# Kernel optimization log

Measured on AMD Instinct MI355X. Metric: run time of the kernel, lower is better.

Reference implementation:

```python
import jax, jax.numpy as jnp
import numpy as np

WS = 8        # window_size
NH = 12       # num_heads


def setup_inputs() -> dict:
    key = jax.random.key(0)
    ks = jax.random.split(key, 9)
    B, C, H, W = 4, 384, 128, 128
    s = 1.0 / np.sqrt(C)
    x = jax.random.normal(ks[0], (B, C, H, W), dtype=jnp.float32)
    Wq = jax.random.normal(ks[1], (C, C), dtype=jnp.float32) * s
    bq = jax.random.normal(ks[2], (C,), dtype=jnp.float32) * 0.01
    Wk = jax.random.normal(ks[3], (C, C), dtype=jnp.float32) * s
    bk = jax.random.normal(ks[4], (C,), dtype=jnp.float32) * 0.01
    Wv = jax.random.normal(ks[5], (C, C), dtype=jnp.float32) * s
    bv = jax.random.normal(ks[6], (C,), dtype=jnp.float32) * 0.01
    Wp = jax.random.normal(ks[7], (C, C), dtype=jnp.float32) * s
    bp = jax.random.normal(ks[8], (C,), dtype=jnp.float32) * 0.01
    return {"x": x, "Wq": Wq, "bq": bq, "Wk": Wk, "bk": bk,
            "Wv": Wv, "bv": bv, "Wp": Wp, "bp": bp}


def reference(x, Wq, bq, Wk, bk, Wv, bv, Wp, bp):
    B, C, H, W = x.shape
    ws2 = WS * WS
    dk = C // NH
    scale = dk ** -0.5

    # window_partition: flat row-major reshape (same semantics as torch's
    # reshape on a contiguous [B,C,H,W] tensor), then permute+view.
    p = x.reshape(B, H // WS, WS, W // WS, WS, C)
    p = jnp.transpose(p, (0, 5, 1, 3, 2, 4))          # [B, C, H/ws, W/ws, ws, ws]
    p = p.reshape(B, C, -1, ws2)                       # [B, C, nW, ws*ws]

    def conv1x1(w, b):  # 1x1 Conv2d on [B,C,nW,ws2]
        return jnp.einsum('bcnw,oc->bonw', p, w) + b[None, :, None, None]

    def heads(t):  # permute(0,2,3,1).contiguous().reshape -> [B, NH, nW, ws2, dk]
        t = jnp.transpose(t, (0, 2, 3, 1))             # [B, nW, ws2, C]
        return t.reshape(B, NH, -1, ws2, dk)           # row-major reinterpretation

    q = heads(conv1x1(Wq, bq))
    k = heads(conv1x1(Wk, bk))
    v = heads(conv1x1(Wv, bv))

    scores = jnp.einsum('bhnqd,bhnkd->bhnqk', q, k) * scale
    attn = jax.nn.softmax(scores, axis=-1)
    o = jnp.einsum('bhnqk,bhnkd->bhnqd', attn, v)      # [B, NH, nW, ws2, dk]
    o = o.reshape(B, -1, ws2, C)                       # [B, nW, ws2, C]

    # window_unpartition
    u = o.reshape(B, -1, WS, WS, C)
    u = jnp.transpose(u, (0, 4, 1, 2, 3))              # [B, C, nW, ws, ws]
    u = u.reshape(B, C, H, W)

    y = jnp.einsum('bchw,oc->bohw', u, Wp) + bp[None, :, None, None]
    return y
```

## Files before the change

### kernel.cpp

```cpp
#include <hip/hip_runtime.h>
#include <hip/hip_bf16.h>
#include <stdint.h>


typedef __bf16 bf16_t;
typedef __bf16 bf16x8 __attribute__((ext_vector_type(8)));
typedef __bf16 bf16x4 __attribute__((ext_vector_type(4)));
typedef float f32x4 __attribute__((ext_vector_type(4)));

__device__ __forceinline__ void gload_lds16(const void* g, void* l) {
  __builtin_amdgcn_global_load_lds((__attribute__((address_space(1))) void*)(g),
                                   (__attribute__((address_space(3))) void*)(l),
                                   16, 0, 0);
}

__global__ __launch_bounds__(256) void convw_kernel(
    const float* __restrict__ wq, const float* __restrict__ wk,
    const float* __restrict__ wv, const float* __restrict__ wp,
    bf16_t* __restrict__ oq, bf16_t* __restrict__ ok,
    bf16_t* __restrict__ ov, bf16_t* __restrict__ op_) {
  int i = blockIdx.x * 256 + threadIdx.x;
  oq[i] = (bf16_t)wq[i];
  ok[i] = (bf16_t)wk[i];
  ov[i] = (bf16_t)wv[i];
  op_[i] = (bf16_t)wp[i];
}

__global__ __launch_bounds__(256) void prep_kernel(const float* __restrict__ x,
                                                   bf16_t* __restrict__ Xp) {
  int gid = blockIdx.x * 256 + threadIdx.x;
  int row = gid / 96;
  int c4 = (gid - row * 96) * 4;
  int b = row >> 14;
  int pp = row & 16383;
  int n1 = pp >> 10, n3 = (pp >> 6) & 15, w2 = (pp >> 3) & 7, w4 = pp & 7;
  int P = (n1 << 10) | (w2 << 7) | (n3 << 3) | w4;
  float4 v = *(const float4*)(x + (size_t)((b << 14) | P) * 384 + c4);
  bf16x4 o;
  o[0] = (bf16_t)v.x; o[1] = (bf16_t)v.y; o[2] = (bf16_t)v.z; o[3] = (bf16_t)v.w;
  *(bf16x4*)(Xp + (size_t)row * 384 + c4) = o;
}

__global__ __launch_bounds__(256) void qkv_gemm(
    const bf16_t* __restrict__ Xp, const bf16_t* __restrict__ Wcat,
    const float* __restrict__ bq, const float* __restrict__ bk,
    const float* __restrict__ bv,
    bf16_t* __restrict__ Qs, bf16_t* __restrict__ Ks, bf16_t* __restrict__ Vs) {
  __shared__ __align__(16) bf16_t As[2 * 256 * 32];
  __shared__ __align__(16) bf16_t Bs[2 * 128 * 32];
  const int tid = threadIdx.x;
  const int F = blockIdx.x;
  const int xcd = F & 7;
  const int t = F >> 3;
  const int j = t % 9;
  const int gq = t / 9;
  const int m0 = (gq * 8 + xcd) * 256;
  const int which = j / 3;
  const int cb = (j % 3) * 128;
  const float* bias = which == 0 ? bq : (which == 1 ? bk : bv);
  bf16_t* Out = which == 0 ? Qs : (which == 1 ? Ks : Vs);
  const bf16_t* Arows = Xp + (size_t)m0 * 384;
  const bf16_t* Brows = Wcat + (size_t)j * 128 * 384;

  const int lane = tid & 63, wvv = tid >> 6;
  const int l15 = lane & 15, hi = lane >> 4;
  const int wrM = wvv >> 1, wc = wvv & 1;
  const int slot = hi ^ ((l15 >> 1) & 3);

  auto stage = [&](int kt) {
    const int k0 = kt * 32;
    bf16_t* Ad = As + (kt & 1) * 8192;
    bf16_t* Bd = Bs + (kt & 1) * 4096;
#pragma unroll
    for (int jj = 0; jj < 4; ++jj) {
      int idx = jj * 256 + tid;
      int row = idx >> 2;
      int sg = (idx & 3) ^ ((idx >> 3) & 3);
      gload_lds16(Arows + (size_t)row * 384 + k0 + sg * 8,
                  (char*)Ad + (jj * 256 + wvv * 64) * 16);
    }
#pragma unroll
    for (int h = 0; h < 2; ++h) {
      int q = wvv * 128 + h * 64 + lane;
      int row = q >> 2;
      int sg = (lane & 3) ^ ((lane >> 3) & 3);
      gload_lds16(Brows + (size_t)row * 384 + k0 + sg * 8,
                  (char*)Bd + (wvv * 128 + h * 64) * 16);
    }
  };

  stage(0);
  stage(1);

  f32x4 acc[8][4] = {};
#pragma unroll 1
  for (int kt = 0; kt < 12; ++kt) {
    bf16_t* Ab = As + (kt & 1) * 8192;
    bf16_t* Bb = Bs + (kt & 1) * 4096;
    if (kt == 11) asm volatile("s_waitcnt vmcnt(0)" ::: "memory");
    else          asm volatile("s_waitcnt vmcnt(6)" ::: "memory");
    __builtin_amdgcn_s_barrier();
    bf16x8 a[8], bfr[4];
#pragma unroll
    for (int i = 0; i < 8; ++i)
      a[i] = *(const bf16x8*)(Ab + (wrM * 128 + i * 16 + l15) * 32 + slot * 8);
#pragma unroll
    for (int ni = 0; ni < 4; ++ni)
      bfr[ni] = *(const bf16x8*)(Bb + (wc * 64 + ni * 16 + l15) * 32 + slot * 8);
#pragma unroll
    for (int mi = 0; mi < 8; ++mi)
#pragma unroll
      for (int ni = 0; ni < 4; ++ni)
        acc[mi][ni] = __builtin_amdgcn_mfma_f32_16x16x32_bf16(a[mi], bfr[ni],
                                                              acc[mi][ni], 0, 0, 0);
    asm volatile("s_waitcnt lgkmcnt(0)" ::: "memory");
    __builtin_amdgcn_sched_barrier(0);
    __builtin_amdgcn_s_barrier();
    if (kt + 2 < 12) stage(kt + 2);
  }

#pragma unroll
  for (int ni = 0; ni < 4; ++ni) {
    int chan = cb + wc * 64 + ni * 16 + l15;
    float bv_ = bias[chan];
#pragma unroll
    for (int mi = 0; mi < 8; ++mi)
#pragma unroll
      for (int r = 0; r < 4; ++r) {
        int row = m0 + wrM * 128 + mi * 16 + hi * 4 + r;
        Out[(size_t)row * 384 + chan] = (bf16_t)(acc[mi][ni][r] + bv_);
      }
  }
}

__global__ __launch_bounds__(64) void attn_kernel(const bf16_t* __restrict__ Q,
                                                  const bf16_t* __restrict__ K,
                                                  const bf16_t* __restrict__ V,
                                                  bf16_t* __restrict__ O) {
  const size_t base = (size_t)blockIdx.x * 2048;
  const bf16_t* q = Q + base;
  const bf16_t* k = K + base;
  const bf16_t* v = V + base;
  bf16_t* o = O + base;
  const int lane = threadIdx.x;
  const int l15 = lane & 15, hi = lane >> 4;

  __shared__ __align__(16) bf16_t Vt[32][72];
  __shared__ __align__(16) bf16_t Ps[64][72];

#pragma unroll
  for (int j = 0; j < 4; ++j) {
    bf16x8 vv = *(const bf16x8*)(v + lane * 32 + j * 8);
#pragma unroll
    for (int e = 0; e < 8; ++e) Vt[j * 8 + e][lane] = vv[e];
  }

  bf16x8 aQ[4], bK[4];
#pragma unroll
  for (int i = 0; i < 4; ++i) {
    aQ[i] = *(const bf16x8*)(q + (i * 16 + l15) * 32 + hi * 8);
    bK[i] = *(const bf16x8*)(k + (i * 16 + l15) * 32 + hi * 8);
  }
  f32x4 sc[4][4] = {};
#pragma unroll
  for (int mi = 0; mi < 4; ++mi)
#pragma unroll
    for (int ni = 0; ni < 4; ++ni)
      sc[mi][ni] = __builtin_amdgcn_mfma_f32_16x16x32_bf16(aQ[mi], bK[ni],
                                                           sc[mi][ni], 0, 0, 0);

  const float SCALE = 0.17677669529663687f;
  float rs[4][4];
#pragma unroll
  for (int mi = 0; mi < 4; ++mi) {
#pragma unroll
    for (int r = 0; r < 4; ++r) {
      float s0 = sc[mi][0][r] * SCALE, s1 = sc[mi][1][r] * SCALE;
      float s2 = sc[mi][2][r] * SCALE, s3 = sc[mi][3][r] * SCALE;
      float mx = fmaxf(fmaxf(s0, s1), fmaxf(s2, s3));
      mx = fmaxf(mx, __shfl_xor(mx, 1));
      mx = fmaxf(mx, __shfl_xor(mx, 2));
      mx = fmaxf(mx, __shfl_xor(mx, 4));
      mx = fmaxf(mx, __shfl_xor(mx, 8));
      float p0 = __expf(s0 - mx), p1 = __expf(s1 - mx);
      float p2 = __expf(s2 - mx), p3 = __expf(s3 - mx);
      int row = mi * 16 + hi * 4 + r;
      Ps[row][0 + l15] = (bf16_t)p0;
      Ps[row][16 + l15] = (bf16_t)p1;
      Ps[row][32 + l15] = (bf16_t)p2;
      Ps[row][48 + l15] = (bf16_t)p3;
      float sum = p0 + p1 + p2 + p3;
      sum += __shfl_xor(sum, 1);
      sum += __shfl_xor(sum, 2);
      sum += __shfl_xor(sum, 4);
      sum += __shfl_xor(sum, 8);
      rs[mi][r] = sum;
    }
  }
  __syncthreads();

  f32x4 oacc[4][2] = {};
#pragma unroll
  for (int mi = 0; mi < 4; ++mi)
#pragma unroll
    for (int ks = 0; ks < 2; ++ks) {
      bf16x8 aP = *(const bf16x8*)(&Ps[mi * 16 + l15][ks * 32 + hi * 8]);
#pragma unroll
      for (int n2 = 0; n2 < 2; ++n2) {
        bf16x8 bV = *(const bf16x8*)(&Vt[n2 * 16 + l15][ks * 32 + hi * 8]);
        oacc[mi][n2] = __builtin_amdgcn_mfma_f32_16x16x32_bf16(aP, bV,
                                                               oacc[mi][n2], 0, 0, 0);
      }
    }
#pragma unroll
  for (int mi = 0; mi < 4; ++mi)
#pragma unroll
    for (int n2 = 0; n2 < 2; ++n2)
#pragma unroll
      for (int r = 0; r < 4; ++r) {
        int row = mi * 16 + hi * 4 + r;
        o[row * 32 + n2 * 16 + l15] = (bf16_t)(oacc[mi][n2][r] / rs[mi][r]);
      }
}

__device__ __forceinline__ void stage_tile(const bf16_t* __restrict__ A,
                                           const bf16_t* __restrict__ B,
                                           bf16_t* As, bf16_t* Bs, int k0, int tid) {
  const int lane = tid & 63, wvv = tid >> 6;
  const int s = (lane & 3) ^ ((lane >> 3) & 3);
#pragma unroll
  for (int j = 0; j < 2; ++j) {
    int q = wvv * 128 + j * 64 + lane;
    int row = q >> 2;
    gload_lds16(A + (size_t)row * 384 + k0 + s * 8,
                (char*)As + (wvv * 128 + j * 64) * 16);
    gload_lds16(B + (size_t)row * 384 + k0 + s * 8,
                (char*)Bs + (wvv * 128 + j * 64) * 16);
  }
}

__device__ __forceinline__ void gemm_mainloop(const bf16_t* __restrict__ Arows,
                                              const bf16_t* __restrict__ Brows,
                                              bf16_t* As, bf16_t* Bs,
                                              int tid, f32x4 acc[4][4]) {
  const int lane = tid & 63;
  const int l15 = lane & 15, hi = lane >> 4;
  const int wr = (tid >> 6) >> 1, wc = (tid >> 6) & 1;
  const int slot = hi ^ ((l15 >> 1) & 3);
  stage_tile(Arows, Brows, As, Bs, 0, tid);
  stage_tile(Arows, Brows, As + 4096, Bs + 4096, 32, tid);
#pragma unroll
  for (int kt = 0; kt < 12; ++kt) {
    bf16_t* Ab = As + (kt & 1) * 4096;
    bf16_t* Bb = Bs + (kt & 1) * 4096;
    if (kt == 11) asm volatile("s_waitcnt vmcnt(0)" ::: "memory");
    else          asm volatile("s_waitcnt vmcnt(4)" ::: "memory");
    __builtin_amdgcn_s_barrier();
    bf16x8 a[4], bfr[4];
#pragma unroll
    for (int i = 0; i < 4; ++i) {
      a[i] = *(const bf16x8*)(Ab + (wr * 64 + i * 16 + l15) * 32 + slot * 8);
      bfr[i] = *(const bf16x8*)(Bb + (wc * 64 + i * 16 + l15) * 32 + slot * 8);
    }
#pragma unroll
    for (int mi = 0; mi < 4; ++mi)
#pragma unroll
      for (int ni = 0; ni < 4; ++ni)
        acc[mi][ni] = __builtin_amdgcn_mfma_f32_16x16x32_bf16(a[mi], bfr[ni],
                                                              acc[mi][ni], 0, 0, 0);
    asm volatile("s_waitcnt lgkmcnt(0)" ::: "memory");
    __builtin_amdgcn_sched_barrier(0);
    __builtin_amdgcn_s_barrier();
    if (kt + 2 < 12)
      stage_tile(Arows, Brows, Ab, Bb, (kt + 2) * 32, tid);
  }
}

__global__ __launch_bounds__(256) void proj_gemm(const bf16_t* __restrict__ Wpb,
                                                 const bf16_t* __restrict__ O,
                                                 const float* __restrict__ bp,
                                                 float* __restrict__ y) {
  __shared__ __align__(16) bf16_t As[2 * 128 * 32];
  __shared__ __align__(16) bf16_t Bs[2 * 128 * 32];
  const int tid = threadIdx.x;
  const int F = blockIdx.x;
  const int xcd = F & 7;
  const int t = F >> 3;
  const int j = t % 3;
  const int gq = t / 3;
  const int g = gq * 8 + xcd;
  const int n0 = (g & 127) * 128;
  const int b = g >> 7;
  const int m0 = j * 128;
  f32x4 acc[4][4] = {};
  gemm_mainloop(Wpb + (size_t)m0 * 384, O + ((size_t)b * 16384 + n0) * 384,
                As, Bs, tid, acc);
  const int lane = tid & 63, wvv = tid >> 6;
  const int l15 = lane & 15, hi = lane >> 4;
  const int wr = wvv >> 1, wc = wvv & 1;
  float* yb = y + (size_t)b * 6291456;
#pragma unroll
  for (int mi = 0; mi < 4; ++mi)
#pragma unroll
    for (int r = 0; r < 4; ++r) {
      int och = m0 + wr * 64 + mi * 16 + hi * 4 + r;
      float bpv = bp[och];
#pragma unroll
      for (int ni = 0; ni < 4; ++ni) {
        int pix = n0 + wc * 64 + ni * 16 + l15;
        yb[(size_t)och * 16384 + pix] = acc[mi][ni][r] + bpv;
      }
    }
}

extern "C" void kernel_launch(void* const* d_in, const int* in_sizes, int n_in,
                              void* d_out, int out_size, void* d_ws, size_t ws_size,
                              hipStream_t stream) {
  const float* x  = (const float*)d_in[0];
  const float* Wq = (const float*)d_in[1];
  const float* bq = (const float*)d_in[2];
  const float* Wk = (const float*)d_in[3];
  const float* bk = (const float*)d_in[4];
  const float* Wv = (const float*)d_in[5];
  const float* bv = (const float*)d_in[6];
  const float* Wp = (const float*)d_in[7];
  const float* bp = (const float*)d_in[8];
  float* y = (float*)d_out;

  char* ws = (char*)d_ws;
  const size_t SZ = 50331648;
  bf16_t* Xp  = (bf16_t*)(ws);
  bf16_t* Vs  = (bf16_t*)(ws + SZ);
  bf16_t* Wcat = (bf16_t*)(ws + 2 * SZ);
  bf16_t* Wkb = Wcat + 147456;
  bf16_t* Wvb = Wkb + 147456;
  bf16_t* Wpb = Wvb + 147456;
  bf16_t* Qs  = (bf16_t*)d_out;
  bf16_t* Ks  = (bf16_t*)((char*)d_out + SZ);
  bf16_t* Ob  = Xp;

  convw_kernel<<<576, 256, 0, stream>>>(Wq, Wk, Wv, Wp, Wcat, Wkb, Wvb, Wpb);
  prep_kernel<<<24576, 256, 0, stream>>>(x, Xp);
  qkv_gemm<<<2304, 256, 0, stream>>>(Xp, Wcat, bq, bk, bv, Qs, Ks, Vs);
  attn_kernel<<<12288, 64, 0, stream>>>(Qs, Ks, Vs, Ob);
  proj_gemm<<<1536, 256, 0, stream>>>(Wpb, Ob, bp, y);
}
```

Baseline: 223.4 us.

## Deepen qkv GEMM pipeline with 5-stage LDS ring and 8 waves

The QKV projection GEMM moves from 256 to 512 threads. Each of its 8 waves now computes a 64x64 sub-tile, where each of the previous 4 waves computed 128x64. The two-stage static LDS double buffer becomes a 5-stage ring in 120KB of dynamic shared memory with 4 stages prefetched ahead. LDS fragments are double-buffered in registers so the next k-step's reads overlap the current MFMAs, and s_setprio is raised around the MFMA block. The aim is to hide global-load latency and cut barrier stalls, at the cost of limiting the kernel to one block per CU because of the large LDS footprint.

```diff
diff --git a/kernel.cpp b/kernel.cpp
--- a/kernel.cpp
+++ b/kernel.cpp
@@ -41,13 +41,12 @@
   *(bf16x4*)(Xp + (size_t)row * 384 + c4) = o;
 }
 
-__global__ __launch_bounds__(256) void qkv_gemm(
+__global__ __launch_bounds__(512, 2) void qkv_gemm(
     const bf16_t* __restrict__ Xp, const bf16_t* __restrict__ Wcat,
     const float* __restrict__ bq, const float* __restrict__ bk,
     const float* __restrict__ bv,
     bf16_t* __restrict__ Qs, bf16_t* __restrict__ Ks, bf16_t* __restrict__ Vs) {
-  __shared__ __align__(16) bf16_t As[2 * 256 * 32];
-  __shared__ __align__(16) bf16_t Bs[2 * 128 * 32];
+  extern __shared__ __align__(16) char smem[];
   const int tid = threadIdx.x;
   const int F = blockIdx.x;
   const int xcd = F & 7;
@@ -62,61 +61,75 @@
   const bf16_t* Arows = Xp + (size_t)m0 * 384;
   const bf16_t* Brows = Wcat + (size_t)j * 128 * 384;
 
-  const int lane = tid & 63, wvv = tid >> 6;
+  const int lane = tid & 63, wid = tid >> 6;
   const int l15 = lane & 15, hi = lane >> 4;
-  const int wrM = wvv >> 1, wc = wvv & 1;
+  const int wr = wid >> 1, wc = wid & 1;
   const int slot = hi ^ ((l15 >> 1) & 3);
 
   auto stage = [&](int kt) {
     const int k0 = kt * 32;
-    bf16_t* Ad = As + (kt & 1) * 8192;
-    bf16_t* Bd = Bs + (kt & 1) * 4096;
-#pragma unroll
-    for (int jj = 0; jj < 4; ++jj) {
-      int idx = jj * 256 + tid;
+    char* base = smem + (kt % 5) * 24576;
+#pragma unroll
+    for (int jj = 0; jj < 2; ++jj) {
+      int idx = jj * 512 + tid;
       int row = idx >> 2;
       int sg = (idx & 3) ^ ((idx >> 3) & 3);
       gload_lds16(Arows + (size_t)row * 384 + k0 + sg * 8,
-                  (char*)Ad + (jj * 256 + wvv * 64) * 16);
-    }
-#pragma unroll
-    for (int h = 0; h < 2; ++h) {
-      int q = wvv * 128 + h * 64 + lane;
-      int row = q >> 2;
-      int sg = (lane & 3) ^ ((lane >> 3) & 3);
+                  base + (jj * 512 + wid * 64) * 16);
+    }
+    {
+      int row = tid >> 2;
+      int sg = (tid & 3) ^ ((tid >> 3) & 3);
       gload_lds16(Brows + (size_t)row * 384 + k0 + sg * 8,
-                  (char*)Bd + (wvv * 128 + h * 64) * 16);
+                  base + 16384 + (wid * 64) * 16);
     }
   };
 
-  stage(0);
-  stage(1);
-
-  f32x4 acc[8][4] = {};
-#pragma unroll 1
+  stage(0); stage(1); stage(2); stage(3);
+  asm volatile("s_waitcnt vmcnt(6)" ::: "memory");
+  __builtin_amdgcn_s_barrier();
+  __builtin_amdgcn_sched_barrier(0);
+
+  bf16x8 fA[2][4], fB[2][4];
+  {
+    const char* Ab = smem;
+    const char* Bb = Ab + 16384;
+#pragma unroll
+    for (int i = 0; i < 4; ++i) {
+      fA[0][i] = *(const bf16x8*)(Ab + (wr * 64 + i * 16 + l15) * 64 + slot * 16);
+      fB[0][i] = *(const bf16x8*)(Bb + (wc * 64 + i * 16 + l15) * 64 + slot * 16);
+    }
+  }
+
+  f32x4 acc[4][4] = {};
+#pragma unroll
   for (int kt = 0; kt < 12; ++kt) {
-    bf16_t* Ab = As + (kt & 1) * 8192;
-    bf16_t* Bb = Bs + (kt & 1) * 4096;
-    if (kt == 11) asm volatile("s_waitcnt vmcnt(0)" ::: "memory");
-    else          asm volatile("s_waitcnt vmcnt(6)" ::: "memory");
-    __builtin_amdgcn_s_barrier();
-    bf16x8 a[8], bfr[4];
-#pragma unroll
-    for (int i = 0; i < 8; ++i)
-      a[i] = *(const bf16x8*)(Ab + (wrM * 128 + i * 16 + l15) * 32 + slot * 8);
-#pragma unroll
-    for (int ni = 0; ni < 4; ++ni)
-      bfr[ni] = *(const bf16x8*)(Bb + (wc * 64 + ni * 16 + l15) * 32 + slot * 8);
-#pragma unroll
-    for (int mi = 0; mi < 8; ++mi)
+    const int cur = kt & 1, nxt = cur ^ 1;
+    if (kt > 0) {
+      __builtin_amdgcn_s_barrier();
+      __builtin_amdgcn_sched_barrier(0);
+    }
+    if (kt + 4 < 12) stage(kt + 4);
+    if (kt < 11) {
+      const char* Ab = smem + ((kt + 1) % 5) * 24576;
+      const char* Bb = Ab + 16384;
+#pragma unroll
+      for (int i = 0; i < 4; ++i) {
+        fA[nxt][i] = *(const bf16x8*)(Ab + (wr * 64 + i * 16 + l15) * 64 + slot * 16);
+        fB[nxt][i] = *(const bf16x8*)(Bb + (wc * 64 + i * 16 + l15) * 64 + slot * 16);
+      }
+    }
+    __builtin_amdgcn_s_setprio(1);
+#pragma unroll
+    for (int mi = 0; mi < 4; ++mi)
 #pragma unroll
       for (int ni = 0; ni < 4; ++ni)
-        acc[mi][ni] = __builtin_amdgcn_mfma_f32_16x16x32_bf16(a[mi], bfr[ni],
-                                                              acc[mi][ni], 0, 0, 0);
-    asm volatile("s_waitcnt lgkmcnt(0)" ::: "memory");
-    __builtin_amdgcn_sched_barrier(0);
-    __builtin_amdgcn_s_barrier();
-    if (kt + 2 < 12) stage(kt + 2);
+        acc[mi][ni] = __builtin_amdgcn_mfma_f32_16x16x32_bf16(
+            fA[cur][mi], fB[cur][ni], acc[mi][ni], 0, 0, 0);
+    __builtin_amdgcn_s_setprio(0);
+    if (kt <= 7)      asm volatile("s_waitcnt vmcnt(6)" ::: "memory");
+    else if (kt == 8) asm volatile("s_waitcnt vmcnt(3)" ::: "memory");
+    else if (kt == 9) asm volatile("s_waitcnt vmcnt(0)" ::: "memory");
   }
 
 #pragma unroll
@@ -124,10 +137,10 @@
     int chan = cb + wc * 64 + ni * 16 + l15;
     float bv_ = bias[chan];
 #pragma unroll
-    for (int mi = 0; mi < 8; ++mi)
+    for (int mi = 0; mi < 4; ++mi)
 #pragma unroll
       for (int r = 0; r < 4; ++r) {
-        int row = m0 + wrM * 128 + mi * 16 + hi * 4 + r;
+        int row = m0 + wr * 64 + mi * 16 + hi * 4 + r;
         Out[(size_t)row * 384 + chan] = (bf16_t)(acc[mi][ni][r] + bv_);
       }
   }
@@ -339,9 +352,12 @@
   bf16_t* Ks  = (bf16_t*)((char*)d_out + SZ);
   bf16_t* Ob  = Xp;
 
+  hipFuncSetAttribute((const void*)qkv_gemm,
+                      hipFuncAttributeMaxDynamicSharedMemorySize, 122880);
+
   convw_kernel<<<576, 256, 0, stream>>>(Wq, Wk, Wv, Wp, Wcat, Wkb, Wvb, Wpb);
   prep_kernel<<<24576, 256, 0, stream>>>(x, Xp);
-  qkv_gemm<<<2304, 256, 0, stream>>>(Xp, Wcat, bq, bk, bv, Qs, Ks, Vs);
+  qkv_gemm<<<2304, 512, 122880, stream>>>(Xp, Wcat, bq, bk, bv, Qs, Ks, Vs);
   attn_kernel<<<12288, 64, 0, stream>>>(Qs, Ks, Vs, Ob);
   proj_gemm<<<1536, 256, 0, stream>>>(Wpb, Ob, bp, y);
 }
```

Measured after the change: 192.1 us. 14.0% less time.

## Triple-buffer QKV GEMM with 512-thread blocks and one barrier per k-step

Applied to the files above, without the earlier changes.

The QKV GEMM now runs 512-thread blocks, each computing a 512x128 output tile instead of 256x128. Shared memory moves to a dynamic, triple-buffered layout, so the next-but-one tile's global-to-LDS loads are issued right after a single barrier per k-step, replacing the two barriers and the full lgkm drain of the old double-buffered loop. The k-loop is fully unrolled and MFMA sections get raised wave priority to overlap loads with math. The cost is 120 KB of LDS per block, which limits each CU to one block, and half as many blocks in the grid.

```diff
diff --git a/kernel.cpp b/kernel.cpp
--- a/kernel.cpp
+++ b/kernel.cpp
@@ -41,20 +41,19 @@
   *(bf16x4*)(Xp + (size_t)row * 384 + c4) = o;
 }
 
-__global__ __launch_bounds__(256) void qkv_gemm(
+__global__ __launch_bounds__(512, 2) void qkv_gemm(
     const bf16_t* __restrict__ Xp, const bf16_t* __restrict__ Wcat,
     const float* __restrict__ bq, const float* __restrict__ bk,
     const float* __restrict__ bv,
     bf16_t* __restrict__ Qs, bf16_t* __restrict__ Ks, bf16_t* __restrict__ Vs) {
-  __shared__ __align__(16) bf16_t As[2 * 256 * 32];
-  __shared__ __align__(16) bf16_t Bs[2 * 128 * 32];
+  extern __shared__ __align__(16) char smem[];
   const int tid = threadIdx.x;
   const int F = blockIdx.x;
   const int xcd = F & 7;
   const int t = F >> 3;
   const int j = t % 9;
   const int gq = t / 9;
-  const int m0 = (gq * 8 + xcd) * 256;
+  const int m0 = (gq * 8 + xcd) * 512;
   const int which = j / 3;
   const int cb = (j % 3) * 128;
   const float* bias = which == 0 ? bq : (which == 1 ? bk : bv);
@@ -62,61 +61,63 @@
   const bf16_t* Arows = Xp + (size_t)m0 * 384;
   const bf16_t* Brows = Wcat + (size_t)j * 128 * 384;
 
-  const int lane = tid & 63, wvv = tid >> 6;
+  const int lane = tid & 63, wid = tid >> 6;
   const int l15 = lane & 15, hi = lane >> 4;
-  const int wrM = wvv >> 1, wc = wvv & 1;
+  const int wr = wid >> 1, wc = wid & 1;
   const int slot = hi ^ ((l15 >> 1) & 3);
 
   auto stage = [&](int kt) {
     const int k0 = kt * 32;
-    bf16_t* Ad = As + (kt & 1) * 8192;
-    bf16_t* Bd = Bs + (kt & 1) * 4096;
+    char* base = smem + (kt % 3) * 40960;
 #pragma unroll
     for (int jj = 0; jj < 4; ++jj) {
-      int idx = jj * 256 + tid;
+      int idx = jj * 512 + tid;
       int row = idx >> 2;
       int sg = (idx & 3) ^ ((idx >> 3) & 3);
       gload_lds16(Arows + (size_t)row * 384 + k0 + sg * 8,
-                  (char*)Ad + (jj * 256 + wvv * 64) * 16);
-    }
-#pragma unroll
-    for (int h = 0; h < 2; ++h) {
-      int q = wvv * 128 + h * 64 + lane;
-      int row = q >> 2;
-      int sg = (lane & 3) ^ ((lane >> 3) & 3);
+                  base + (jj * 512 + wid * 64) * 16);
+    }
+    {
+      int row = tid >> 2;
+      int sg = (tid & 3) ^ ((tid >> 3) & 3);
       gload_lds16(Brows + (size_t)row * 384 + k0 + sg * 8,
-                  (char*)Bd + (wvv * 128 + h * 64) * 16);
+                  base + 32768 + (wid * 64) * 16);
     }
   };
 
-  stage(0);
-  stage(1);
+  stage(0); stage(1);
+  asm volatile("s_waitcnt vmcnt(5)" ::: "memory");
+  __builtin_amdgcn_s_barrier();
+  __builtin_amdgcn_sched_barrier(0);
 
   f32x4 acc[8][4] = {};
-#pragma unroll 1
+#pragma unroll
   for (int kt = 0; kt < 12; ++kt) {
-    bf16_t* Ab = As + (kt & 1) * 8192;
-    bf16_t* Bb = Bs + (kt & 1) * 4096;
-    if (kt == 11) asm volatile("s_waitcnt vmcnt(0)" ::: "memory");
-    else          asm volatile("s_waitcnt vmcnt(6)" ::: "memory");
-    __builtin_amdgcn_s_barrier();
+    if (kt > 0) {
+      __builtin_amdgcn_s_barrier();
+      __builtin_amdgcn_sched_barrier(0);
+    }
+    if (kt + 2 < 12) stage(kt + 2);
+    const char* Ab = smem + (kt % 3) * 40960;
+    const char* Bb = Ab + 32768;
     bf16x8 a[8], bfr[4];
 #pragma unroll
     for (int i = 0; i < 8; ++i)
-      a[i] = *(const bf16x8*)(Ab + (wrM * 128 + i * 16 + l15) * 32 + slot * 8);
+      a[i] = *(const bf16x8*)(Ab + (wr * 128 + i * 16 + l15) * 64 + slot * 16);
 #pragma unroll
     for (int ni = 0; ni < 4; ++ni)
-      bfr[ni] = *(const bf16x8*)(Bb + (wc * 64 + ni * 16 + l15) * 32 + slot * 8);
+      bfr[ni] = *(const bf16x8*)(Bb + (wc * 64 + ni * 16 + l15) * 64 + slot * 16);
+    __builtin_amdgcn_s_setprio(1);
 #pragma unroll
     for (int mi = 0; mi < 8; ++mi)
 #pragma unroll
       for (int ni = 0; ni < 4; ++ni)
         acc[mi][ni] = __builtin_amdgcn_mfma_f32_16x16x32_bf16(a[mi], bfr[ni],
                                                               acc[mi][ni], 0, 0, 0);
-    asm volatile("s_waitcnt lgkmcnt(0)" ::: "memory");
+    __builtin_amdgcn_s_setprio(0);
+    if (kt <= 9)       asm volatile("s_waitcnt vmcnt(5)" ::: "memory");
+    else if (kt == 10) asm volatile("s_waitcnt vmcnt(0)" ::: "memory");
     __builtin_amdgcn_sched_barrier(0);
-    __builtin_amdgcn_s_barrier();
-    if (kt + 2 < 12) stage(kt + 2);
   }
 
 #pragma unroll
@@ -127,7 +128,7 @@
     for (int mi = 0; mi < 8; ++mi)
 #pragma unroll
       for (int r = 0; r < 4; ++r) {
-        int row = m0 + wrM * 128 + mi * 16 + hi * 4 + r;
+        int row = m0 + wr * 128 + mi * 16 + hi * 4 + r;
         Out[(size_t)row * 384 + chan] = (bf16_t)(acc[mi][ni][r] + bv_);
       }
   }
@@ -339,9 +340,12 @@
   bf16_t* Ks  = (bf16_t*)((char*)d_out + SZ);
   bf16_t* Ob  = Xp;
 
+  hipFuncSetAttribute((const void*)qkv_gemm,
+                      hipFuncAttributeMaxDynamicSharedMemorySize, 122880);
+
   convw_kernel<<<576, 256, 0, stream>>>(Wq, Wk, Wv, Wp, Wcat, Wkb, Wvb, Wpb);
   prep_kernel<<<24576, 256, 0, stream>>>(x, Xp);
-  qkv_gemm<<<2304, 256, 0, stream>>>(Xp, Wcat, bq, bk, bv, Qs, Ks, Vs);
+  qkv_gemm<<<1152, 512, 122880, stream>>>(Xp, Wcat, bq, bk, bv, Qs, Ks, Vs);
   attn_kernel<<<12288, 64, 0, stream>>>(Qs, Ks, Vs, Ob);
   proj_gemm<<<1536, 256, 0, stream>>>(Wpb, Ob, bp, y);
 }
```

After: 197.5 us. 1.13x faster.
